# Kernel tuning notes

Measured on AMD Instinct MI355X. Metric: run time of the kernel, lower is better.

## Reference

```python
import jax, jax.numpy as jnp
import numpy as np

N_NODES = 100000
N_EDGES = 3200000
N_GRAPHS = 1000
IN_DIM = 10
HID = 20
N_CLASSES = 2
BN_EPS = 1e-5


def setup_inputs() -> dict:
    key = jax.random.key(0)
    ks = jax.random.split(key, 12)
    x = jax.random.normal(ks[0], (N_NODES, IN_DIM), dtype=jnp.float32)
    edge_index = jax.random.randint(ks[1], (2, N_EDGES), 0, N_NODES, dtype=jnp.int64)
    batch = jnp.sort(jax.random.randint(ks[2], (N_NODES,), 0, N_GRAPHS, dtype=jnp.int64))
    def lin(k, fan_in, fan_out):
        bound = 1.0 / np.sqrt(fan_in)
        kw, kb = jax.random.split(k)
        W = jax.random.uniform(kw, (fan_in, fan_out), jnp.float32, -bound, bound)
        b = jax.random.uniform(kb, (fan_out,), jnp.float32, -bound, bound)
        return W, b
    W1, b1 = lin(ks[3], IN_DIM, HID)
    W2, b2 = lin(ks[4], HID, HID)
    W3, b3 = lin(ks[5], HID, HID)
    fcW, fcb = lin(ks[6], HID, N_CLASSES)
    ones = jnp.ones((HID,), jnp.float32)
    zeros = jnp.zeros((HID,), jnp.float32)
    return {
        "x": x, "edge_index": edge_index, "batch": batch,
        "W1": W1, "b1": b1, "g1": ones, "beta1": zeros,
        "W2": W2, "b2": b2, "g2": ones, "beta2": zeros,
        "W3": W3, "b3": b3, "g3": ones, "beta3": zeros,
        "fcW": fcW, "fcb": fcb,
    }


def _gin_layer(h, src, dst, W, b, g, beta):
    # GIN aggregation: (1+eps)*x_i + sum_{j->i} x_j, eps = 0
    agg = jax.ops.segment_sum(h[src], dst, num_segments=N_NODES)  # [N, d]
    h = (h + agg) @ W + b                                          # MLP (single Linear)
    mu = jnp.mean(h, axis=0)                                       # BatchNorm (batch stats)
    var = jnp.mean(jnp.square(h - mu), axis=0)
    h = (h - mu) * jax.lax.rsqrt(var + BN_EPS) * g + beta
    return jax.nn.relu(h)                                          # dropout p=0 is identity


def reference(x, edge_index, batch, W1, b1, g1, beta1, W2, b2, g2, beta2,
              W3, b3, g3, beta3, fcW, fcb):
    src, dst = edge_index[0], edge_index[1]
    h = _gin_layer(x, src, dst, W1, b1, g1, beta1)
    h = _gin_layer(h, src, dst, W2, b2, g2, beta2)
    h = _gin_layer(h, src, dst, W3, b3, g3, beta3)
    graph_emb = jax.ops.segment_sum(h, batch, num_segments=N_GRAPHS)  # global add pool
    return graph_emb @ fcW + fcb
```

## Files before the change

### kernel.cpp

```cpp
#include <hip/hip_runtime.h>
#include <hip/hip_bf16.h>
#include <hip/hip_fp16.h>

#define N_NODES  100000
#define N_EDGES  3200000
#define N_GRAPHS 1000
#define IN_DIM   10
#define HID      20
#define BN_EPS   1e-5f

#define BSH   8
#define NB    ((N_NODES + 255) / 256)
#define CAP   9216
#define FB    256
#define FCHUNK ((N_EDGES + FB - 1) / FB)
#define NBG   ((N_NODES + 31) / 32)

__global__ __launch_bounds__(512) void fill_direct(const int* __restrict__ src,
                                                   const int* __restrict__ dst,
                                                   int* __restrict__ bcur,
                                                   unsigned* __restrict__ packed) {
    __shared__ int sdst[FCHUNK];
    __shared__ int cnt[NB];
    __shared__ int base[NB];
    int t = threadIdx.x;
    for (int i = t; i < NB; i += 512) cnt[i] = 0;
    __syncthreads();
    int e0 = blockIdx.x * FCHUNK;
    int e1 = min(e0 + FCHUNK, N_EDGES);
    int m = e1 - e0;
    for (int i = t; i < m; i += 512) {
        int d = dst[e0 + i];
        sdst[i] = d;
        atomicAdd(&cnt[d >> BSH], 1);
    }
    __syncthreads();
    for (int i = t; i < NB; i += 512) {
        int c = cnt[i];
        base[i] = c ? atomicAdd(&bcur[i], c) : 0;
        cnt[i] = 0;
    }
    __syncthreads();
    for (int i = t; i < m; i += 512) {
        int d = sdst[i];
        int b = d >> BSH;
        int r = atomicAdd(&cnt[b], 1);
        packed[(size_t)b * CAP + base[b] + r] =
            (unsigned)src[e0 + i] | ((unsigned)(d & 255) << 24);
    }
}

__global__ void scan_buckets(const int* __restrict__ bcur, int* __restrict__ off) {
    __shared__ int lds[512];
    int t = threadIdx.x;
    int v = (t < NB) ? bcur[t] : 0;
    int val = v;
    lds[t] = val; __syncthreads();
    for (int o = 1; o < 512; o <<= 1) {
        int a = (t >= o) ? lds[t - o] : 0;
        __syncthreads();
        val += a; lds[t] = val;
        __syncthreads();
    }
    if (t < NB) off[t] = val - v;
    if (t == 0) off[NB] = N_EDGES;
}

__global__ __launch_bounds__(512) void sort_bucket(const unsigned* __restrict__ packed,
                                                   const int* __restrict__ bcnt,
                                                   const int* __restrict__ off,
                                                   int* __restrict__ csr,
                                                   int* __restrict__ rp) {
    __shared__ unsigned ebuf[CAP];
    __shared__ int cnt[256];
    __shared__ int cur[256];
    int b = blockIdx.x, t = threadIdx.x;
    int m = bcnt[b];
    int o = off[b];
    const unsigned* pb = packed + (size_t)b * CAP;
    for (int i = t; i < m; i += 512) ebuf[i] = pb[i];
    if (t < 256) cnt[t] = 0;
    __syncthreads();
    for (int i = t; i < m; i += 512) atomicAdd(&cnt[ebuf[i] >> 24], 1);
    __syncthreads();
    int v = 0, val = 0;
    if (t < 256) { v = cnt[t]; val = v; cur[t] = val; }
    __syncthreads();
    for (int ofs = 1; ofs < 256; ofs <<= 1) {
        int add = (t < 256 && t >= ofs) ? cur[t - ofs] : 0;
        __syncthreads();
        if (t < 256) { val += add; cur[t] = val; }
        __syncthreads();
    }
    if (t < 256) {
        int node = b * 256 + t;
        if (node <= N_NODES) rp[node] = o + (val - v);
        cur[t] = val - v;
    }
    __syncthreads();
    for (int i = t; i < m; i += 512) {
        unsigned p = ebuf[i];
        int l = p >> 24;
        int pos = atomicAdd(&cur[l], 1);
        csr[o + pos] = (int)(p & 0xFFFFFFu);
    }
}

__global__ void split_x(const float* __restrict__ x,
                        float* __restrict__ xlo, float* __restrict__ xhi) {
    int n = blockIdx.x * blockDim.x + threadIdx.x;
    if (n >= N_NODES) return;
    const float2* xp = (const float2*)(x + (size_t)n * 10);
    float2 v0 = xp[0], v1 = xp[1], v2 = xp[2], v3 = xp[3], v4 = xp[4];
    float4* lp = (float4*)(xlo + (size_t)n * 8);
    float4 a; a.x = v0.x; a.y = v0.y; a.z = v1.x; a.w = v1.y;
    float4 b; b.x = v2.x; b.y = v2.y; b.z = v3.x; b.w = v3.y;
    lp[0] = a; lp[1] = b;
    *(float2*)(xhi + (size_t)n * 2) = v4;
}

template<int DIN, bool BN>
__global__ __launch_bounds__(256) void gather_mlp8(
        const float* __restrict__ flo, const float* __restrict__ fhi,
        const __half* __restrict__ hlo, const __half* __restrict__ hhi,
        const int* __restrict__ rp, const int* __restrict__ csr,
        const float* __restrict__ W,
        const float* __restrict__ bias,
        const float* __restrict__ ssin,
        __half* __restrict__ olo,
        __half* __restrict__ ohi,
        float* __restrict__ partials)
{
    __shared__ float sW[DIN * HID];
    __shared__ float sb[HID];
    __shared__ float sss[2 * HID];
    __shared__ float red[4][2 * HID];
    __shared__ __half sh[32][24];
    int t = threadIdx.x;
    for (int i = t; i < DIN * HID; i += 256) sW[i] = W[i];
    if (t < HID) sb[t] = bias[t];
    if constexpr (BN) { if (t < 2 * HID) sss[t] = ssin[t]; }
    __syncthreads();

    int node = blockIdx.x * 32 + (t >> 3);
    int sub  = t & 7;
    float u[DIN];
#pragma unroll
    for (int k = 0; k < DIN; k++) u[k] = 0.0f;

    auto acch2 = [&](unsigned w, int q) {
        __half2 h2 = *(const __half2*)&w;
        float2 f = __half22float2(h2);
        float v0 = f.x, v1 = f.y;
        if constexpr (BN) {
            v0 = fmaxf(fmaf(v0, sss[2*q+0], sss[HID+2*q+0]), 0.f);
            v1 = fmaxf(fmaf(v1, sss[2*q+1], sss[HID+2*q+1]), 0.f);
        }
        u[2*q] += v0; u[2*q+1] += v1;
    };
    auto accrow20 = [&](uint4 A, uint4 B, uint2 C) {
        acch2(A.x, 0); acch2(A.y, 1); acch2(A.z, 2); acch2(A.w, 3);
        acch2(B.x, 4); acch2(B.y, 5); acch2(B.z, 6); acch2(B.w, 7);
        acch2(C.x, 8); acch2(C.y, 9);
    };

    if (node < N_NODES) {
        int e0 = rp[node], e1 = rp[node + 1];
        if constexpr (DIN == 20) {
            if (sub == 0) {
                const uint4* l = (const uint4*)(hlo + (size_t)node * 16);
                uint4 A = l[0], B = l[1];
                uint2 C = *(const uint2*)(hhi + (size_t)node * 4);
                accrow20(A, B, C);
            }
            int e = e0 + sub;
            for (; e + 8 < e1; e += 16) {
                int s0 = csr[e], s1 = csr[e + 8];
                const uint4* l0 = (const uint4*)(hlo + (size_t)s0 * 16);
                const uint4* l1 = (const uint4*)(hlo + (size_t)s1 * 16);
                uint4 A0 = l0[0], B0 = l0[1];
                uint2 C0 = *(const uint2*)(hhi + (size_t)s0 * 4);
                uint4 A1 = l1[0], B1 = l1[1];
                uint2 C1 = *(const uint2*)(hhi + (size_t)s1 * 4);
                accrow20(A0, B0, C0);
                accrow20(A1, B1, C1);
            }
            if (e < e1) {
                int s0 = csr[e];
                const uint4* l0 = (const uint4*)(hlo + (size_t)s0 * 16);
                uint4 A = l0[0], B = l0[1];
                uint2 C = *(const uint2*)(hhi + (size_t)s0 * 4);
                accrow20(A, B, C);
            }
        } else {
            auto accrow10 = [&](float4 A, float4 B, float2 C) {
                u[0] += A.x; u[1] += A.y; u[2] += A.z; u[3] += A.w;
                u[4] += B.x; u[5] += B.y; u[6] += B.z; u[7] += B.w;
                u[8] += C.x; u[9] += C.y;
            };
            if (sub == 0) {
                const float4* l = (const float4*)(flo + (size_t)node * 8);
                accrow10(l[0], l[1], *(const float2*)(fhi + (size_t)node * 2));
            }
            int e = e0 + sub;
            for (; e + 8 < e1; e += 16) {
                int s0 = csr[e], s1 = csr[e + 8];
                const float4* l0 = (const float4*)(flo + (size_t)s0 * 8);
                const float4* l1 = (const float4*)(flo + (size_t)s1 * 8);
                float4 A0 = l0[0], B0 = l0[1];
                float2 C0 = *(const float2*)(fhi + (size_t)s0 * 2);
                float4 A1 = l1[0], B1 = l1[1];
                float2 C1 = *(const float2*)(fhi + (size_t)s1 * 2);
                accrow10(A0, B0, C0);
                accrow10(A1, B1, C1);
            }
            if (e < e1) {
                int s0 = csr[e];
                const float4* l0 = (const float4*)(flo + (size_t)s0 * 8);
                accrow10(l0[0], l0[1], *(const float2*)(fhi + (size_t)s0 * 2));
            }
        }
    }

#pragma unroll
    for (int k = 0; k < DIN; k++) {
        u[k] += __shfl_xor(u[k], 1);
        u[k] += __shfl_xor(u[k], 2);
        u[k] += __shfl_xor(u[k], 4);
    }

    const int c0 = (sub & 3) * 5;
    float out[5];
#pragma unroll
    for (int j = 0; j < 5; j++) out[j] = sb[c0 + j];
#pragma unroll
    for (int k = 0; k < DIN; k++) {
        float uk = u[k];
#pragma unroll
        for (int j = 0; j < 5; j++)
            out[j] = fmaf(uk, sW[k * HID + c0 + j], out[j]);
    }
    bool live = (node < N_NODES) && (sub < 4);
    if (live) {
        int nl = t >> 3;
#pragma unroll
        for (int j = 0; j < 5; j++) sh[nl][c0 + j] = __float2half(out[j]);
    }

    float msk = live ? 1.0f : 0.0f;
    float s1[5], s2[5];
#pragma unroll
    for (int j = 0; j < 5; j++) {
        float o = out[j] * msk;
        s1[j] = o; s2[j] = o * out[j];
    }
    for (int o = 8; o < 64; o <<= 1) {
#pragma unroll
        for (int j = 0; j < 5; j++) {
            s1[j] += __shfl_down(s1[j], o);
            s2[j] += __shfl_down(s2[j], o);
        }
    }
    int lane = t & 63, wave = t >> 6;
    if (lane < 4) {
#pragma unroll
        for (int j = 0; j < 5; j++) {
            red[wave][lane * 5 + j]       = s1[j];
            red[wave][HID + lane * 5 + j] = s2[j];
        }
    }
    __syncthreads();
    if (t < 32) {
        int n2 = blockIdx.x * 32 + t;
        if (n2 < N_NODES) {
            const uint4* sp = (const uint4*)&sh[t][0];
            uint4 a0 = sp[0], a1 = sp[1];
            uint2 a2 = *(const uint2*)&sh[t][16];
            uint4* lp = (uint4*)(olo + (size_t)n2 * 16);
            lp[0] = a0; lp[1] = a1;
            *(uint2*)(ohi + (size_t)n2 * 4) = a2;
        }
    }
    if (t < 2 * HID)
        partials[(size_t)t * NBG + blockIdx.x] =
            red[0][t] + red[1][t] + red[2][t] + red[3][t];
}

__global__ __launch_bounds__(256) void bn_prep(const float* __restrict__ partials,
                                               const float* __restrict__ g,
                                               const float* __restrict__ beta,
                                               float* __restrict__ ss) {
    int c = blockIdx.x, t = threadIdx.x;
    double a1 = 0.0, a2 = 0.0;
    for (int i = t; i < NBG; i += 256) {
        a1 += (double)partials[(size_t)c * NBG + i];
        a2 += (double)partials[(size_t)(c + HID) * NBG + i];
    }
    for (int o = 32; o; o >>= 1) {
        a1 += __shfl_down(a1, o);
        a2 += __shfl_down(a2, o);
    }
    __shared__ double r1[4], r2[4];
    int lane = t & 63, wave = t >> 6;
    if (lane == 0) { r1[wave] = a1; r2[wave] = a2; }
    __syncthreads();
    if (t == 0) {
        double su = r1[0] + r1[1] + r1[2] + r1[3];
        double sq = r2[0] + r2[1] + r2[2] + r2[3];
        double mu  = su / (double)N_NODES;
        double var = sq / (double)N_NODES - mu * mu;
        float sc = g[c] * (float)(1.0 / sqrt(var + (double)BN_EPS));
        ss[c]       = sc;
        ss[HID + c] = beta[c] - (float)mu * sc;
    }
}

__global__ void gptr_kernel(const int* __restrict__ batch, int* __restrict__ gptr) {
    int n = blockIdx.x * blockDim.x + threadIdx.x;
    if (n >= N_NODES) return;
    int g = batch[n];
    int gp = (n == 0) ? -1 : batch[n - 1];
    for (int q = gp + 1; q <= g; q++) gptr[q] = n;
    if (n == N_NODES - 1)
        for (int q = g + 1; q <= N_GRAPHS; q++) gptr[q] = N_NODES;
}

__global__ __launch_bounds__(256) void pool_fc(const __half* __restrict__ hlo,
                                               const __half* __restrict__ hhi,
                                               const int* __restrict__ gptr,
                                               const float* __restrict__ ss,
                                               const float* __restrict__ fcW,
                                               const float* __restrict__ fcb,
                                               float* __restrict__ out) {
    __shared__ float red[12][HID];
    __shared__ float sss[2 * HID];
    __shared__ float pl[HID];
    int g = blockIdx.x, t = threadIdx.x;
    if (t < 2 * HID) sss[t] = ss[t];
    __syncthreads();
    int n0 = gptr[g], n1 = gptr[g + 1];
    if (t < 240) {
        int c = t % HID, grp = t / HID;
        float s = 0.0f;
        for (int n = n0 + grp; n < n1; n += 12) {
            float raw = (c < 16) ? __half2float(hlo[(size_t)n * 16 + c])
                                 : __half2float(hhi[(size_t)n * 4 + (c - 16)]);
            float v = fmaf(raw, sss[c], sss[HID + c]);
            s += v > 0.0f ? v : 0.0f;
        }
        red[grp][c] = s;
    }
    __syncthreads();
    if (t < HID) {
        float a = 0.0f;
#pragma unroll
        for (int q = 0; q < 12; q++) a += red[q][t];
        pl[t] = a;
    }
    __syncthreads();
    if (t < 2) {
        float o = fcb[t];
#pragma unroll
        for (int k = 0; k < HID; k++) o = fmaf(pl[k], fcW[k * 2 + t], o);
        out[g * 2 + t] = o;
    }
}

extern "C" void kernel_launch(void* const* d_in, const int* in_sizes, int n_in,
                              void* d_out, int out_size, void* d_ws, size_t ws_size,
                              hipStream_t stream) {
    const float* x     = (const float*)d_in[0];
    const int*   eidx  = (const int*)d_in[1];
    const int*   batch = (const int*)d_in[2];
    const float* W1 = (const float*)d_in[3];
    const float* b1 = (const float*)d_in[4];
    const float* g1 = (const float*)d_in[5];
    const float* be1 = (const float*)d_in[6];
    const float* W2 = (const float*)d_in[7];
    const float* b2 = (const float*)d_in[8];
    const float* g2 = (const float*)d_in[9];
    const float* be2 = (const float*)d_in[10];
    const float* W3 = (const float*)d_in[11];
    const float* b3 = (const float*)d_in[12];
    const float* g3 = (const float*)d_in[13];
    const float* be3 = (const float*)d_in[14];
    const float* fcW = (const float*)d_in[15];
    const float* fcb = (const float*)d_in[16];
    float* out = (float*)d_out;

    const int* src = eidx;
    const int* dst = eidx + N_EDGES;

    char* ws = (char*)d_ws;
    __half* hAlo   = (__half*)(ws + 0);
    __half* hAhi   = (__half*)(ws + 3200000);
    __half* hBlo   = (__half*)(ws + 4000000);
    __half* hBhi   = (__half*)(ws + 7200000);
    float*  xlo    = (float*)(ws + 8000000);
    float*  xhi    = (float*)(ws + 11200000);
    unsigned* packed = (unsigned*)(ws + 0);
    int*   csr     = (int*)(ws + 16000000);
    int*   rp      = (int*)(ws + 28800000);
    int*   off     = (int*)(ws + 29200128);
    int*   bcur    = (int*)(ws + 29203328);
    float* partials= (float*)(ws + 29209728);
    float* ss1     = (float*)(ws + 29709728);
    float* ss2     = (float*)(ws + 29709888);
    float* ss3     = (float*)(ws + 29710048);
    int*   gptr    = (int*)(ws + 29710208);

    const int BLK = 256;

    hipMemsetAsync(bcur, 0, NB * sizeof(int), stream);
    fill_direct<<<FB, 512, 0, stream>>>(src, dst, bcur, packed);
    scan_buckets<<<1, 512, 0, stream>>>(bcur, off);
    sort_bucket<<<NB, 512, 0, stream>>>(packed, bcur, off, csr, rp);
    gptr_kernel<<<(N_NODES + BLK - 1) / BLK, BLK, 0, stream>>>(batch, gptr);
    split_x<<<(N_NODES + BLK - 1) / BLK, BLK, 0, stream>>>(x, xlo, xhi);

    gather_mlp8<IN_DIM, false><<<NBG, BLK, 0, stream>>>(xlo, xhi,
        (const __half*)nullptr, (const __half*)nullptr,
        rp, csr, W1, b1, ss1, hAlo, hAhi, partials);
    bn_prep<<<HID, BLK, 0, stream>>>(partials, g1, be1, ss1);

    gather_mlp8<HID, true><<<NBG, BLK, 0, stream>>>((const float*)nullptr,
        (const float*)nullptr, hAlo, hAhi,
        rp, csr, W2, b2, ss1, hBlo, hBhi, partials);
    bn_prep<<<HID, BLK, 0, stream>>>(partials, g2, be2, ss2);

    gather_mlp8<HID, true><<<NBG, BLK, 0, stream>>>((const float*)nullptr,
        (const float*)nullptr, hBlo, hBhi,
        rp, csr, W3, b3, ss2, hAlo, hAhi, partials);
    bn_prep<<<HID, BLK, 0, stream>>>(partials, g3, be3, ss3);

    pool_fc<<<N_GRAPHS, BLK, 0, stream>>>(hAlo, hAhi, gptr, ss3, fcW, fcb, out);
}
```

Before: 326.4 us.

## Fold bucket scan and graph-pointer build into sort_bucket; add nontemporal loads

Removes the separate single-block scan_buckets and gptr_kernel launches. Each sort_bucket block now works out its own bucket offset with a wave-shuffle reduction over the preceding bucket counts, and it also fills the graph pointer array for its 256 nodes. Nontemporal loads are used for the streaming src/dst reads and the packed-bucket reads. This saves two launches and the serialization they add, at the cost of every block redundantly reading up to NB counts. It relies on NB (391) being at most 512.

```diff
diff --git a/kernel.cpp b/kernel.cpp
--- a/kernel.cpp
+++ b/kernel.cpp
@@ -15,6 +15,8 @@
 #define FB    256
 #define FCHUNK ((N_EDGES + FB - 1) / FB)
 #define NBG   ((N_NODES + 31) / 32)
+
+#define NTL(p) __builtin_nontemporal_load(p)
 
 __global__ __launch_bounds__(512) void fill_direct(const int* __restrict__ src,
                                                    const int* __restrict__ dst,
@@ -30,7 +32,7 @@
     int e1 = min(e0 + FCHUNK, N_EDGES);
     int m = e1 - e0;
     for (int i = t; i < m; i += 512) {
-        int d = dst[e0 + i];
+        int d = NTL(dst + e0 + i);
         sdst[i] = d;
         atomicAdd(&cnt[d >> BSH], 1);
     }
@@ -46,39 +48,52 @@
         int b = d >> BSH;
         int r = atomicAdd(&cnt[b], 1);
         packed[(size_t)b * CAP + base[b] + r] =
-            (unsigned)src[e0 + i] | ((unsigned)(d & 255) << 24);
-    }
-}
-
-__global__ void scan_buckets(const int* __restrict__ bcur, int* __restrict__ off) {
-    __shared__ int lds[512];
-    int t = threadIdx.x;
-    int v = (t < NB) ? bcur[t] : 0;
-    int val = v;
-    lds[t] = val; __syncthreads();
-    for (int o = 1; o < 512; o <<= 1) {
-        int a = (t >= o) ? lds[t - o] : 0;
-        __syncthreads();
-        val += a; lds[t] = val;
-        __syncthreads();
-    }
-    if (t < NB) off[t] = val - v;
-    if (t == 0) off[NB] = N_EDGES;
+            (unsigned)NTL(src + e0 + i) | ((unsigned)(d & 255) << 24);
+    }
 }
 
 __global__ __launch_bounds__(512) void sort_bucket(const unsigned* __restrict__ packed,
                                                    const int* __restrict__ bcnt,
-                                                   const int* __restrict__ off,
                                                    int* __restrict__ csr,
-                                                   int* __restrict__ rp) {
+                                                   int* __restrict__ rp,
+                                                   const int* __restrict__ batch,
+                                                   int* __restrict__ gptr) {
     __shared__ unsigned ebuf[CAP];
     __shared__ int cnt[256];
     __shared__ int cur[256];
+    __shared__ int wsum[8];
+    __shared__ int s_off;
     int b = blockIdx.x, t = threadIdx.x;
     int m = bcnt[b];
-    int o = off[b];
+
+    {
+        int v = (t < b) ? bcnt[t] : 0;
+        for (int o = 32; o; o >>= 1) v += __shfl_down(v, o);
+        if ((t & 63) == 0) wsum[t >> 6] = v;
+        __syncthreads();
+        if (t == 0) {
+            int s = 0;
+#pragma unroll
+            for (int i = 0; i < 8; i++) s += wsum[i];
+            s_off = s;
+        }
+        __syncthreads();
+    }
+    int o = s_off;
+
+    if (t < 256) {
+        int n = b * 256 + t;
+        if (n < N_NODES) {
+            int g = batch[n];
+            int gp = (n == 0) ? -1 : batch[n - 1];
+            for (int q = gp + 1; q <= g; q++) gptr[q] = n;
+            if (n == N_NODES - 1)
+                for (int q = g + 1; q <= N_GRAPHS; q++) gptr[q] = N_NODES;
+        }
+    }
+
     const unsigned* pb = packed + (size_t)b * CAP;
-    for (int i = t; i < m; i += 512) ebuf[i] = pb[i];
+    for (int i = t; i < m; i += 512) ebuf[i] = NTL(pb + i);
     if (t < 256) cnt[t] = 0;
     __syncthreads();
     for (int i = t; i < m; i += 512) atomicAdd(&cnt[ebuf[i] >> 24], 1);
@@ -163,6 +178,11 @@
         acch2(B.x, 4); acch2(B.y, 5); acch2(B.z, 6); acch2(B.w, 7);
         acch2(C.x, 8); acch2(C.y, 9);
     };
+    auto accrow10 = [&](float4 A, float4 B, float2 C) {
+        u[0] += A.x; u[1] += A.y; u[2] += A.z; u[3] += A.w;
+        u[4] += B.x; u[5] += B.y; u[6] += B.z; u[7] += B.w;
+        u[8] += C.x; u[9] += C.y;
+    };
 
     if (node < N_NODES) {
         int e0 = rp[node], e1 = rp[node + 1];
@@ -193,11 +213,6 @@
                 accrow20(A, B, C);
             }
         } else {
-            auto accrow10 = [&](float4 A, float4 B, float2 C) {
-                u[0] += A.x; u[1] += A.y; u[2] += A.z; u[3] += A.w;
-                u[4] += B.x; u[5] += B.y; u[6] += B.z; u[7] += B.w;
-                u[8] += C.x; u[9] += C.y;
-            };
             if (sub == 0) {
                 const float4* l = (const float4*)(flo + (size_t)node * 8);
                 accrow10(l[0], l[1], *(const float2*)(fhi + (size_t)node * 2));
@@ -313,16 +328,6 @@
         ss[c]       = sc;
         ss[HID + c] = beta[c] - (float)mu * sc;
     }
-}
-
-__global__ void gptr_kernel(const int* __restrict__ batch, int* __restrict__ gptr) {
-    int n = blockIdx.x * blockDim.x + threadIdx.x;
-    if (n >= N_NODES) return;
-    int g = batch[n];
-    int gp = (n == 0) ? -1 : batch[n - 1];
-    for (int q = gp + 1; q <= g; q++) gptr[q] = n;
-    if (n == N_NODES - 1)
-        for (int q = g + 1; q <= N_GRAPHS; q++) gptr[q] = N_NODES;
 }
 
 __global__ __launch_bounds__(256) void pool_fc(const __half* __restrict__ hlo,
@@ -401,7 +406,6 @@
     unsigned* packed = (unsigned*)(ws + 0);
     int*   csr     = (int*)(ws + 16000000);
     int*   rp      = (int*)(ws + 28800000);
-    int*   off     = (int*)(ws + 29200128);
     int*   bcur    = (int*)(ws + 29203328);
     float* partials= (float*)(ws + 29209728);
     float* ss1     = (float*)(ws + 29709728);
@@ -413,9 +417,7 @@
 
     hipMemsetAsync(bcur, 0, NB * sizeof(int), stream);
     fill_direct<<<FB, 512, 0, stream>>>(src, dst, bcur, packed);
-    scan_buckets<<<1, 512, 0, stream>>>(bcur, off);
-    sort_bucket<<<NB, 512, 0, stream>>>(packed, bcur, off, csr, rp);
-    gptr_kernel<<<(N_NODES + BLK - 1) / BLK, BLK, 0, stream>>>(batch, gptr);
+    sort_bucket<<<NB, 512, 0, stream>>>(packed, bcur, csr, rp, batch, gptr);
     split_x<<<(N_NODES + BLK - 1) / BLK, BLK, 0, stream>>>(x, xlo, xhi);
 
     gather_mlp8<IN_DIM, false><<<NBG, BLK, 0, stream>>>(xlo, xhi,
```

After: 336.7 us. +3.2%, slower.
